# Performance work log

Hardware: AMD Instinct MI355X
Metric: run time of the kernel (lower is better)

The kernel has to match this reference:

```python
import jax, jax.numpy as jnp
import numpy as np

B, S, D_MODEL, D_OUT = 4, 4096, 512, 64


def setup_inputs() -> dict:
    key = jax.random.key(0)
    ks = jax.random.split(key, 10)
    query = jax.random.normal(ks[0], (B, S, D_MODEL), dtype=jnp.float32)
    key_t = jax.random.normal(ks[1], (B, S, D_MODEL), dtype=jnp.float32)
    value = jax.random.normal(ks[2], (B, S, D_MODEL), dtype=jnp.float32)
    mask = jax.random.randint(ks[3], (B, S, S), 0, 2, dtype=jnp.int32)
    sc = 1.0 / np.sqrt(D_MODEL)
    Wq = jax.random.uniform(ks[4], (D_MODEL, D_OUT), minval=-sc, maxval=sc, dtype=jnp.float32)
    bq = jnp.zeros((D_OUT,), dtype=jnp.float32)
    Wk = jax.random.uniform(ks[5], (D_MODEL, D_OUT), minval=-sc, maxval=sc, dtype=jnp.float32)
    bk = jnp.zeros((D_OUT,), dtype=jnp.float32)
    Wv = jax.random.uniform(ks[6], (D_MODEL, D_OUT), minval=-sc, maxval=sc, dtype=jnp.float32)
    bv = jnp.zeros((D_OUT,), dtype=jnp.float32)
    return {"query": query, "key": key_t, "value": value, "mask": mask,
            "Wq": Wq, "bq": bq, "Wk": Wk, "bk": bk, "Wv": Wv, "bv": bv}


def reference(query, key, value, mask, Wq, bq, Wk, bk, Wv, bv):
    # Linear projections (single head): [B,S,D_MODEL] @ [D_MODEL,D_OUT] + bias
    q = jnp.einsum('bsd,de->bse', query, Wq) + bq
    k = jnp.einsum('bsd,de->bse', key, Wk) + bk
    v = jnp.einsum('bsd,de->bse', value, Wv) + bv
    dim_k = k.shape[-1]
    scores = jnp.einsum('bqe,bke->bqk', q, k) / jnp.sqrt(jnp.float32(dim_k))  # [B,S,S]
    scores = jnp.where(mask == 0, -jnp.inf, scores)
    weights = jax.nn.softmax(scores, axis=-1)
    # dropout is identity in eval mode / for deterministic reference
    outputs = jnp.einsum('bqk,bke->bqe', weights, v)  # [B,S,D_OUT]
    return outputs
```

## Files before the change

kernel.cpp:

```cpp
#include <hip/hip_runtime.h>
#include <hip/hip_bf16.h>

#define BB 4
#define SS 4096
#define DMODEL 512
#define DOUT 64
#define KSPLIT 4

typedef __bf16 bf16_t;
typedef __bf16 bf16x8 __attribute__((ext_vector_type(8)));
typedef float floatx4 __attribute__((ext_vector_type(4)));

__global__ __launch_bounds__(256) void wtrans_kernel(
    const float* __restrict__ Wq, const float* __restrict__ Wk,
    const float* __restrict__ Wv, bf16_t* __restrict__ wT) {
  int idx = blockIdx.x * 256 + threadIdx.x;
  int mat = idx >> 12;
  int r   = idx & 4095;
  int e   = r & 63;
  int d0  = (r >> 6) << 3;
  const float* W = (mat == 0) ? Wq : ((mat == 1) ? Wk : Wv);
  bf16_t* dst = wT + (size_t)mat * (DOUT * DMODEL) + (size_t)e * DMODEL + d0;
#pragma unroll
  for (int j = 0; j < 8; ++j) dst[j] = (bf16_t)W[(size_t)(d0 + j) * DOUT + e];
}

__global__ __launch_bounds__(256) void proj_kernel(
    const float* __restrict__ inq, const float* __restrict__ ink,
    const float* __restrict__ inv, const bf16_t* __restrict__ wT,
    const float* __restrict__ bq, const float* __restrict__ bk,
    const float* __restrict__ bv,
    bf16_t* __restrict__ q_ws, bf16_t* __restrict__ k_ws,
    bf16_t* __restrict__ v_wsT) {
  const int mat = blockIdx.x >> 8;
  const int s0  = (blockIdx.x & 255) << 6;
  const int lane = threadIdx.x & 63;
  const int w    = threadIdx.x >> 6;
  const int col  = lane & 15, quad = lane >> 4;

  const float* inp  = (mat == 0) ? inq : ((mat == 1) ? ink : inv);
  const float* bias = (mat == 0) ? bq : ((mat == 1) ? bk : bv);
  const bf16_t* wt  = wT + (size_t)mat * (DOUT * DMODEL);

  const int arow = s0 + w * 16 + col;
  floatx4 acc[4] = {};

  for (int ch = 0; ch < 16; ++ch) {
    const int d0 = ch * 32 + quad * 8;
    float4 a0 = *(const float4*)(inp + (size_t)arow * DMODEL + d0);
    float4 a1 = *(const float4*)(inp + (size_t)arow * DMODEL + d0 + 4);
    bf16x8 af;
    af[0] = (bf16_t)a0.x; af[1] = (bf16_t)a0.y; af[2] = (bf16_t)a0.z; af[3] = (bf16_t)a0.w;
    af[4] = (bf16_t)a1.x; af[5] = (bf16_t)a1.y; af[6] = (bf16_t)a1.z; af[7] = (bf16_t)a1.w;
#pragma unroll
    for (int c = 0; c < 4; ++c) {
      bf16x8 bw = *(const bf16x8*)(wt + (size_t)(c * 16 + col) * DMODEL + d0);
      acc[c] = __builtin_amdgcn_mfma_f32_16x16x32_bf16(af, bw, acc[c], 0, 0, 0);
    }
  }

#pragma unroll
  for (int c = 0; c < 4; ++c) {
    float bcol = bias[c * 16 + col];
#pragma unroll
    for (int r = 0; r < 4; ++r) {
      int row = s0 + w * 16 + quad * 4 + r;
      float v = acc[c][r] + bcol;
      if (mat == 2) {
        int b = row >> 12, sp = row & 4095;
        v_wsT[((size_t)(b * DOUT + c * 16 + col)) * SS + sp] = (bf16_t)v;
      } else {
        bf16_t* dst = (mat == 0) ? q_ws : k_ws;
        dst[(size_t)row * DOUT + c * 16 + col] = (bf16_t)v;
      }
    }
  }
}

__global__ __launch_bounds__(1024, 4) void attn_kernel(
    const bf16_t* __restrict__ q_ws, const bf16_t* __restrict__ k_ws,
    const bf16_t* __restrict__ v_wsT, const int* __restrict__ mask,
    float* __restrict__ out) {
  const int b  = blockIdx.x >> 6;
  const int q0 = (blockIdx.x & 63) << 6;
  const int lane = threadIdx.x & 63;
  const int wv   = threadIdx.x >> 6;
  const int g    = wv >> 2;
  const int wi   = wv & 3;
  const int col  = lane & 15, quad = lane >> 4;

  __shared__ __align__(16) char arena[3 * 64 * 66 * 4 + 3 * 64 * 4];
  bf16_t (*Pg)[72] = (bf16_t (*)[72])(arena + (size_t)g * 64 * 72 * 2);
  float* Ored = (float*)arena;
  float* lred = (float*)(arena + 3 * 64 * 66 * 4);

  const int qrowA = q0 + wi * 16 + col;
  const bf16_t* qbase = q_ws + ((size_t)(b * SS) + qrowA) * DOUT + quad * 8;
  const bf16x8 qa0 = *(const bf16x8*)(qbase);
  const bf16x8 qa1 = *(const bf16x8*)(qbase + 32);
  const int* mrow = mask + ((size_t)(b * SS) + qrowA) * SS + quad * 8;

  floatx4 o[4] = {};
  float l_acc = 0.f;

  int4 mc[2][2], mn[2][2];
  auto loadM = [&](int k0, int4 m[2][2]) {
#pragma unroll
    for (int s = 0; s < 2; ++s) {
      const int4* mp = (const int4*)(mrow + k0 + s * 32);
      m[s][0] = mp[0];
      m[s][1] = mp[1];
    }
  };
  loadM(g * 64, mc);

  const bf16_t* prow_r = &Pg[wi * 16 + col][quad * 8];

  const int NIT = SS / (64 * KSPLIT);
  for (int it = 0; it < NIT; ++it) {
    const int k0 = g * 64 + it * (64 * KSPLIT);
    const int k0n = (it + 1 < NIT) ? k0 + 64 * KSPLIT : k0;
    loadM(k0n, mn);

    floatx4 sacc[4];
    {
      bf16x8 kc[4][2];
#pragma unroll
      for (int c = 0; c < 4; ++c)
#pragma unroll
        for (int s = 0; s < 2; ++s)
          kc[c][s] = *(const bf16x8*)(k_ws + ((size_t)(b * SS) + k0 + c * 16 + col) * DOUT + s * 32 + quad * 8);
#pragma unroll
      for (int c = 0; c < 4; ++c) {
        floatx4 z = {};
        z = __builtin_amdgcn_mfma_f32_16x16x32_bf16(qa0, kc[c][0], z, 0, 0, 0);
        z = __builtin_amdgcn_mfma_f32_16x16x32_bf16(qa1, kc[c][1], z, 0, 0, 0);
        sacc[c] = z;
      }
    }

    bf16x8 vc[4][2];
#pragma unroll
    for (int c = 0; c < 4; ++c)
#pragma unroll
      for (int s = 0; s < 2; ++s)
        vc[c][s] = *(const bf16x8*)(v_wsT + ((size_t)(b * DOUT) + c * 16 + col) * SS + k0 + s * 32 + quad * 8);

#pragma unroll
    for (int c = 0; c < 4; ++c)
#pragma unroll
      for (int r = 0; r < 4; ++r)
        Pg[wi * 16 + quad * 4 + r][c * 16 + col] = (bf16_t)__expf(sacc[c][r] * 0.125f);

    asm volatile("s_waitcnt lgkmcnt(0)" ::: "memory");

    bf16x8 pa0 = *(const bf16x8*)(prow_r);
    bf16x8 pa1 = *(const bf16x8*)(prow_r + 32);

    float lp = 0.f;
    bf16x8 pm0, pm1;
    auto apply = [&](bf16x8 pa, int4 mlo, int4 mhi, bf16x8& pm) {
      int mm[8] = {mlo.x, mlo.y, mlo.z, mlo.w, mhi.x, mhi.y, mhi.z, mhi.w};
#pragma unroll
      for (int j = 0; j < 8; ++j) {
        bf16_t pv = (mm[j] != 0) ? pa[j] : (bf16_t)0.0f;
        pm[j] = pv;
        lp += (float)pv;
      }
    };
    apply(pa0, mc[0][0], mc[0][1], pm0);
    apply(pa1, mc[1][0], mc[1][1], pm1);
    lp += __shfl_xor(lp, 16);
    lp += __shfl_xor(lp, 32);
    l_acc += lp;

#pragma unroll
    for (int c = 0; c < 4; ++c) {
      o[c] = __builtin_amdgcn_mfma_f32_16x16x32_bf16(pm0, vc[c][0], o[c], 0, 0, 0);
      o[c] = __builtin_amdgcn_mfma_f32_16x16x32_bf16(pm1, vc[c][1], o[c], 0, 0, 0);
    }

    mc[0][0] = mn[0][0]; mc[0][1] = mn[0][1];
    mc[1][0] = mn[1][0]; mc[1][1] = mn[1][1];
  }

  __syncthreads();
  if (g > 0) {
    float* Og = Ored + (size_t)(g - 1) * 64 * 66;
#pragma unroll
    for (int c = 0; c < 4; ++c)
#pragma unroll
      for (int r = 0; r < 4; ++r)
        Og[(wi * 16 + quad * 4 + r) * 66 + c * 16 + col] = o[c][r];
    if (quad == 0) lred[(g - 1) * 64 + wi * 16 + col] = l_acc;
  }
  __syncthreads();
  if (g == 0) {
#pragma unroll
    for (int p = 0; p < 3; ++p) {
      float* Og = Ored + (size_t)p * 64 * 66;
#pragma unroll
      for (int c = 0; c < 4; ++c)
#pragma unroll
        for (int r = 0; r < 4; ++r)
          o[c][r] += Og[(wi * 16 + quad * 4 + r) * 66 + c * 16 + col];
    }
#pragma unroll
    for (int r = 0; r < 4; ++r) {
      float lr = __shfl(l_acc, quad * 4 + r, 64);
#pragma unroll
      for (int p = 0; p < 3; ++p) lr += lred[p * 64 + wi * 16 + quad * 4 + r];
      float inv_l = 1.0f / lr;
      int row = q0 + wi * 16 + quad * 4 + r;
#pragma unroll
      for (int c = 0; c < 4; ++c)
        out[((size_t)(b * SS) + row) * DOUT + c * 16 + col] = o[c][r] * inv_l;
    }
  }
}

extern "C" void kernel_launch(void* const* d_in, const int* in_sizes, int n_in,
                              void* d_out, int out_size, void* d_ws, size_t ws_size,
                              hipStream_t stream) {
  const float* query = (const float*)d_in[0];
  const float* key   = (const float*)d_in[1];
  const float* value = (const float*)d_in[2];
  const int*   mask  = (const int*)d_in[3];
  const float* Wq = (const float*)d_in[4];
  const float* bq = (const float*)d_in[5];
  const float* Wk = (const float*)d_in[6];
  const float* bk = (const float*)d_in[7];
  const float* Wv = (const float*)d_in[8];
  const float* bv = (const float*)d_in[9];
  float* out = (float*)d_out;

  bf16_t* q_ws  = (bf16_t*)d_ws;
  bf16_t* k_ws  = q_ws + (size_t)BB * SS * DOUT;
  bf16_t* v_wsT = k_ws + (size_t)BB * SS * DOUT;
  bf16_t* wT    = v_wsT + (size_t)BB * SS * DOUT;

  hipLaunchKernelGGL(wtrans_kernel, dim3(48), dim3(256), 0, stream, Wq, Wk, Wv, wT);
  hipLaunchKernelGGL(proj_kernel, dim3(768), dim3(256), 0, stream,
                     query, key, value, wT, bq, bk, bv, q_ws, k_ws, v_wsT);
  hipLaunchKernelGGL(attn_kernel, dim3(256), dim3(1024), 0, stream,
                     q_ws, k_ws, v_wsT, mask, out);
}
```

Before: 517.7 us.

## Pre-pack int32 mask into bitmasks before attention kernel

Adds a kernel that packs the int32 mask into 64-bit ballot bitmasks, and has the attention kernel read one u64 per row chunk instead of 16 ints per lane. This removes the wide mask loads and their registers from the attention inner loop, and moves K and V loads ahead of the score MFMAs. In exchange there is an extra pass over the full mask and another launch.

```diff
diff --git a/kernel.cpp b/kernel.cpp
--- a/kernel.cpp
+++ b/kernel.cpp
@@ -10,6 +10,8 @@
 typedef __bf16 bf16_t;
 typedef __bf16 bf16x8 __attribute__((ext_vector_type(8)));
 typedef float floatx4 __attribute__((ext_vector_type(4)));
+typedef unsigned long long u64;
+typedef u64 u64x2 __attribute__((ext_vector_type(2)));
 
 __global__ __launch_bounds__(256) void wtrans_kernel(
     const float* __restrict__ Wq, const float* __restrict__ Wk,
@@ -23,6 +25,25 @@
   bf16_t* dst = wT + (size_t)mat * (DOUT * DMODEL) + (size_t)e * DMODEL + d0;
 #pragma unroll
   for (int j = 0; j < 8; ++j) dst[j] = (bf16_t)W[(size_t)(d0 + j) * DOUT + e];
+}
+
+__global__ __launch_bounds__(256) void maskpack_kernel(
+    const int* __restrict__ mask, u64* __restrict__ bits) {
+  const int wid  = (blockIdx.x * 256 + threadIdx.x) >> 6;
+  const int lane = threadIdx.x & 63;
+  const int* base = mask + (size_t)wid * 1024;
+  u64* wbase = bits + (size_t)wid * 16;
+#pragma unroll
+  for (int c = 0; c < 4; ++c) {
+    const int* p = base + c * 256;
+    u64 b0 = __ballot(p[lane] != 0);
+    u64 b1 = __ballot(p[lane + 64] != 0);
+    u64 b2 = __ballot(p[lane + 128] != 0);
+    u64 b3 = __ballot(p[lane + 192] != 0);
+    u64x2 w01 = {b0, b1}, w23 = {b2, b3};
+    if (lane == 0) *(u64x2*)(wbase + c * 4) = w01;
+    if (lane == 1) *(u64x2*)(wbase + c * 4 + 2) = w23;
+  }
 }
 
 __global__ __launch_bounds__(256) void proj_kernel(
@@ -79,7 +100,7 @@
 
 __global__ __launch_bounds__(1024, 4) void attn_kernel(
     const bf16_t* __restrict__ q_ws, const bf16_t* __restrict__ k_ws,
-    const bf16_t* __restrict__ v_wsT, const int* __restrict__ mask,
+    const bf16_t* __restrict__ v_wsT, const u64* __restrict__ bits,
     float* __restrict__ out) {
   const int b  = blockIdx.x >> 6;
   const int q0 = (blockIdx.x & 63) << 6;
@@ -98,46 +119,25 @@
   const bf16_t* qbase = q_ws + ((size_t)(b * SS) + qrowA) * DOUT + quad * 8;
   const bf16x8 qa0 = *(const bf16x8*)(qbase);
   const bf16x8 qa1 = *(const bf16x8*)(qbase + 32);
-  const int* mrow = mask + ((size_t)(b * SS) + qrowA) * SS + quad * 8;
+  const u64* brow = bits + ((size_t)(b * SS) + qrowA) * (SS / 64);
 
   floatx4 o[4] = {};
   float l_acc = 0.f;
 
-  int4 mc[2][2], mn[2][2];
-  auto loadM = [&](int k0, int4 m[2][2]) {
-#pragma unroll
-    for (int s = 0; s < 2; ++s) {
-      const int4* mp = (const int4*)(mrow + k0 + s * 32);
-      m[s][0] = mp[0];
-      m[s][1] = mp[1];
-    }
-  };
-  loadM(g * 64, mc);
-
+  u64 bits_cur = brow[g];
   const bf16_t* prow_r = &Pg[wi * 16 + col][quad * 8];
 
   const int NIT = SS / (64 * KSPLIT);
   for (int it = 0; it < NIT; ++it) {
     const int k0 = g * 64 + it * (64 * KSPLIT);
     const int k0n = (it + 1 < NIT) ? k0 + 64 * KSPLIT : k0;
-    loadM(k0n, mn);
-
-    floatx4 sacc[4];
-    {
-      bf16x8 kc[4][2];
-#pragma unroll
-      for (int c = 0; c < 4; ++c)
-#pragma unroll
-        for (int s = 0; s < 2; ++s)
-          kc[c][s] = *(const bf16x8*)(k_ws + ((size_t)(b * SS) + k0 + c * 16 + col) * DOUT + s * 32 + quad * 8);
-#pragma unroll
-      for (int c = 0; c < 4; ++c) {
-        floatx4 z = {};
-        z = __builtin_amdgcn_mfma_f32_16x16x32_bf16(qa0, kc[c][0], z, 0, 0, 0);
-        z = __builtin_amdgcn_mfma_f32_16x16x32_bf16(qa1, kc[c][1], z, 0, 0, 0);
-        sacc[c] = z;
-      }
-    }
+
+    bf16x8 kc[4][2];
+#pragma unroll
+    for (int c = 0; c < 4; ++c)
+#pragma unroll
+      for (int s = 0; s < 2; ++s)
+        kc[c][s] = *(const bf16x8*)(k_ws + ((size_t)(b * SS) + k0 + c * 16 + col) * DOUT + s * 32 + quad * 8);
 
     bf16x8 vc[4][2];
 #pragma unroll
@@ -146,6 +146,17 @@
       for (int s = 0; s < 2; ++s)
         vc[c][s] = *(const bf16x8*)(v_wsT + ((size_t)(b * DOUT) + c * 16 + col) * SS + k0 + s * 32 + quad * 8);
 
+    u64 bits_nxt = brow[k0n >> 6];
+
+    floatx4 sacc[4];
+#pragma unroll
+    for (int c = 0; c < 4; ++c) {
+      floatx4 z = {};
+      z = __builtin_amdgcn_mfma_f32_16x16x32_bf16(qa0, kc[c][0], z, 0, 0, 0);
+      z = __builtin_amdgcn_mfma_f32_16x16x32_bf16(qa1, kc[c][1], z, 0, 0, 0);
+      sacc[c] = z;
+    }
+
 #pragma unroll
     for (int c = 0; c < 4; ++c)
 #pragma unroll
@@ -157,19 +168,19 @@
     bf16x8 pa0 = *(const bf16x8*)(prow_r);
     bf16x8 pa1 = *(const bf16x8*)(prow_r + 32);
 
+    unsigned lo32 = (unsigned)bits_cur;
+    unsigned hi32 = (unsigned)(bits_cur >> 32);
+    unsigned m8a = (lo32 >> (quad * 8)) & 0xffu;
+    unsigned m8b = (hi32 >> (quad * 8)) & 0xffu;
     float lp = 0.f;
     bf16x8 pm0, pm1;
-    auto apply = [&](bf16x8 pa, int4 mlo, int4 mhi, bf16x8& pm) {
-      int mm[8] = {mlo.x, mlo.y, mlo.z, mlo.w, mhi.x, mhi.y, mhi.z, mhi.w};
-#pragma unroll
-      for (int j = 0; j < 8; ++j) {
-        bf16_t pv = (mm[j] != 0) ? pa[j] : (bf16_t)0.0f;
-        pm[j] = pv;
-        lp += (float)pv;
-      }
-    };
-    apply(pa0, mc[0][0], mc[0][1], pm0);
-    apply(pa1, mc[1][0], mc[1][1], pm1);
+#pragma unroll
+    for (int j = 0; j < 8; ++j) {
+      bf16_t p0 = ((m8a >> j) & 1u) ? pa0[j] : (bf16_t)0.0f;
+      bf16_t p1 = ((m8b >> j) & 1u) ? pa1[j] : (bf16_t)0.0f;
+      pm0[j] = p0; pm1[j] = p1;
+      lp += (float)p0 + (float)p1;
+    }
     lp += __shfl_xor(lp, 16);
     lp += __shfl_xor(lp, 32);
     l_acc += lp;
@@ -180,8 +191,7 @@
       o[c] = __builtin_amdgcn_mfma_f32_16x16x32_bf16(pm1, vc[c][1], o[c], 0, 0, 0);
     }
 
-    mc[0][0] = mn[0][0]; mc[0][1] = mn[0][1];
-    mc[1][0] = mn[1][0]; mc[1][1] = mn[1][1];
+    bits_cur = bits_nxt;
   }
 
   __syncthreads();
@@ -238,10 +248,13 @@
   bf16_t* k_ws  = q_ws + (size_t)BB * SS * DOUT;
   bf16_t* v_wsT = k_ws + (size_t)BB * SS * DOUT;
   bf16_t* wT    = v_wsT + (size_t)BB * SS * DOUT;
-
+  u64*    bits  = (u64*)(wT + 3 * DOUT * DMODEL);
+
+  hipLaunchKernelGGL(maskpack_kernel, dim3(BB * SS * SS / 1024 / 4), dim3(256), 0, stream,
+                     mask, bits);
   hipLaunchKernelGGL(wtrans_kernel, dim3(48), dim3(256), 0, stream, Wq, Wk, Wv, wT);
   hipLaunchKernelGGL(proj_kernel, dim3(768), dim3(256), 0, stream,
                      query, key, value, wT, bq, bk, bv, q_ws, k_ws, v_wsT);
   hipLaunchKernelGGL(attn_kernel, dim3(256), dim3(1024), 0, stream,
-                     q_ws, k_ws, v_wsT, mask, out);
-}
+                     q_ws, k_ws, v_wsT, bits, out);
+}
```

Measured after the change: 567.5 us. 9.6% more time.
